# Kernel tuning notes

Hardware: AMD Instinct MI355X
Metric: run time of the kernel (lower is better)

Reference implementation:

```python
import jax, jax.numpy as jnp
import numpy as np

N = 20000   # nodes
E = 320000  # edges
F = 64      # input node features
H = 256     # hidden_layer_size
C = 10      # nbr_classes
G = 64      # graphs in the batch


def _lin(key, fan_in, fan_out):
    k1, k2 = jax.random.split(key)
    bound = 1.0 / np.sqrt(fan_in)
    W = jax.random.uniform(k1, (fan_in, fan_out), jnp.float32, -bound, bound)
    b = jax.random.uniform(k2, (fan_out,), jnp.float32, -bound, bound)
    return W, b


def setup_inputs() -> dict:
    key = jax.random.key(0)
    ks = jax.random.split(key, 10)
    x = jax.random.normal(ks[0], (N, F), jnp.float32)
    edge_index = jax.random.randint(ks[1], (2, E), 0, N)
    batch = jnp.sort(jax.random.randint(ks[2], (N,), 0, G))
    W1, b1 = _lin(ks[3], F, H)
    W2, b2 = _lin(ks[4], H, H)
    W3, b3 = _lin(ks[5], H, H)
    W4, b4 = _lin(ks[6], H, H)
    W5, b5 = _lin(ks[7], H, H)
    Wout, bout = _lin(ks[8], H, C)
    return {"x": x, "edge_index": edge_index, "batch": batch,
            "W1": W1, "b1": b1, "W2": W2, "b2": b2, "W3": W3, "b3": b3,
            "W4": W4, "b4": b4, "W5": W5, "b5": b5, "Wout": Wout, "bout": bout}


def reference(x, edge_index, batch, W1, b1, W2, b2, W3, b3, W4, b4, W5, b5, Wout, bout):
    # GCNConv (Kipf & Welling): add self-loops, D^{-1/2}(A+I)D^{-1/2} (X W) + b.
    # Dropout(p=0.5) is identity in eval mode (reference is deterministic).
    loop = jnp.arange(N)
    row = jnp.concatenate([edge_index[0], loop])  # source nodes, [E+N]
    col = jnp.concatenate([edge_index[1], loop])  # target nodes, [E+N]
    deg = jax.ops.segment_sum(jnp.ones(E + N, x.dtype), col, num_segments=N)
    dinv = jax.lax.rsqrt(deg)  # deg >= 1 thanks to self-loops
    norm = (dinv[row] * dinv[col])[:, None]  # [E+N, 1]

    def gcn_conv(h, W, b):
        m = (h @ W)[row] * norm                      # gather + normalize, [E+N, H]
        return jax.ops.segment_sum(m, col, num_segments=N) + b

    h = x
    for W, b in ((W1, b1), (W2, b2), (W3, b3), (W4, b4), (W5, b5)):
        h = jax.nn.relu(gcn_conv(h, W, b))

    # global_mean_pool over graph ids
    counts = jax.ops.segment_sum(jnp.ones(N, h.dtype), batch, num_segments=G)
    pooled = jax.ops.segment_sum(h, batch, num_segments=G) / jnp.maximum(counts, 1.0)[:, None]
    return pooled @ Wout + bout  # [G, C]
```

## Files before the change

kernel.cpp:

```cpp
#include <hip/hip_runtime.h>

#define NN 20000
#define NE 320000
#define FIN 64
#define HD 256
#define NC 10
#define NG 64
#define NB ((NN + 255) / 256)

typedef unsigned short u16;
typedef unsigned int u32;
typedef __attribute__((ext_vector_type(8))) short short8;
typedef __attribute__((ext_vector_type(4))) float f32x4;

__device__ __forceinline__ float bf2f(u16 u) {
    union { u32 i; float f; } v; v.i = ((u32)u) << 16; return v.f;
}
__device__ __forceinline__ u16 f2bf(float f) {
    union { float f; u32 i; } v; v.f = f;
    u32 r = v.i + 0x7fffu + ((v.i >> 16) & 1u);
    return (u16)(r >> 16);
}

__global__ void k_deg(const int* __restrict__ col, int* __restrict__ degi,
                      const int* __restrict__ batch, int* __restrict__ gstart) {
    int i = blockIdx.x * 256 + threadIdx.x;
    if (i < NE) atomicAdd(&degi[col[i]], 1);
    if (i < NN) {
        int b = batch[i];
        int prev = (i == 0) ? -1 : batch[i - 1];
        if (b != prev) gstart[b] = i;
    }
}

__global__ __launch_bounds__(256) void k_scan1(const int* __restrict__ degi,
                                               int* __restrict__ rowptr,
                                               int* __restrict__ bsum) {
    int t = threadIdx.x;
    int i = blockIdx.x * 256 + t;
    int v = (i < NN) ? degi[i] : 0;
    int lane = t & 63, wid = t >> 6;
    int x = v;
#pragma unroll
    for (int off = 1; off < 64; off <<= 1) {
        int y = __shfl_up(x, off);
        if (lane >= off) x += y;
    }
    __shared__ int ws[4];
    if (lane == 63) ws[wid] = x;
    __syncthreads();
    int woff = 0;
    for (int w = 0; w < wid; ++w) woff += ws[w];
    if (i < NN) rowptr[i] = woff + x - v;
    if (t == 255) bsum[blockIdx.x] = woff + x;
}

__global__ void k_scan3(const int* __restrict__ degi, const int* __restrict__ bsum,
                        int* __restrict__ rowptr, int* __restrict__ cursor,
                        float* __restrict__ dinv,
                        const float* __restrict__ x, u16* __restrict__ u0) {
    __shared__ int pref[NB];
    if (threadIdx.x < NB) pref[threadIdx.x] = bsum[threadIdx.x];
    __syncthreads();
    if (threadIdx.x == 0) {
        int run = 0;
        for (int k = 0; k < NB; ++k) { int t = pref[k]; pref[k] = run; run += t; }
    }
    __syncthreads();
    int i = blockIdx.x * 256 + threadIdx.x;
    if (i < NN) {
        int dg = degi[i];
        int rp = rowptr[i] + pref[i >> 8];
        rowptr[i] = rp;
        cursor[i] = rp;
        dinv[i] = rsqrtf((float)(1 + dg));
        if (i == NN - 1) rowptr[NN] = rp + dg;
    }
    if (i < NN * FIN / 4) {
        int node = i >> 4;
        float d = rsqrtf((float)(1 + degi[node]));
        float4 v = *(const float4*)&x[(size_t)i * 4];
        u32 lo = (u32)f2bf(v.x * d) | ((u32)f2bf(v.y * d) << 16);
        u32 hi = (u32)f2bf(v.z * d) | ((u32)f2bf(v.w * d) << 16);
        *(uint2*)&u0[(size_t)i * 4] = make_uint2(lo, hi);
    }
}

__global__ void k_fill(const int* __restrict__ row, const int* __restrict__ col,
                       int* __restrict__ cursor, int* __restrict__ ebuf) {
    int e = blockIdx.x * 256 + threadIdx.x;
    if (e < NE) {
        int c = col[e];
        int pos = atomicAdd(&cursor[c], 1);
        ebuf[pos] = row[e];
    }
}

__global__ __launch_bounds__(256) void k_trans(const float* __restrict__ W0, const float* __restrict__ W1,
                                               const float* __restrict__ W2, const float* __restrict__ W3,
                                               const float* __restrict__ W4,
                                               u16* __restrict__ T0, u16* __restrict__ T1,
                                               u16* __restrict__ T2, u16* __restrict__ T3,
                                               u16* __restrict__ T4) {
    int l = blockIdx.z;
    const float* W = (l == 0) ? W0 : (l == 1) ? W1 : (l == 2) ? W2 : (l == 3) ? W3 : W4;
    u16* T = (l == 0) ? T0 : (l == 1) ? T1 : (l == 2) ? T2 : (l == 3) ? T3 : T4;
    int K = (l == 0) ? FIN : HD;
    int k0 = blockIdx.x * 32;
    if (k0 >= K) return;
    int n0 = blockIdx.y * 32;
    __shared__ float tile[32][33];
    int tx = threadIdx.x & 31, ty = threadIdx.x >> 5;
#pragma unroll
    for (int r = 0; r < 32; r += 8)
        tile[ty + r][tx] = W[(size_t)(k0 + ty + r) * HD + n0 + tx];
    __syncthreads();
#pragma unroll
    for (int r = 0; r < 32; r += 8)
        T[(size_t)(n0 + ty + r) * K + k0 + tx] = f2bf(tile[tx][ty + r]);
}

__global__ __launch_bounds__(256) void k_gatherh(const u16* __restrict__ U,
                                                 const int* __restrict__ rowptr,
                                                 const int* __restrict__ ebuf,
                                                 const float* __restrict__ dinv,
                                                 u16* __restrict__ Z) {
    int b = blockIdx.x;
    int half = b & 1;
    int tile = b >> 1;
    int n = tile * 4 + (threadIdx.x >> 6);
    if (n >= NN) return;
    int lane = threadIdx.x & 63;
    int grp = lane >> 4;
    int seg = lane & 15;
    int fbase = half * 128 + seg * 8;
    int s = rowptr[n], e = rowptr[n + 1];
    float acc[8];
    if (grp == 0) {
        uint4 v = *(const uint4*)&U[(size_t)n * HD + fbase];
        acc[0] = bf2f((u16)(v.x & 0xffff)); acc[1] = bf2f((u16)(v.x >> 16));
        acc[2] = bf2f((u16)(v.y & 0xffff)); acc[3] = bf2f((u16)(v.y >> 16));
        acc[4] = bf2f((u16)(v.z & 0xffff)); acc[5] = bf2f((u16)(v.z >> 16));
        acc[6] = bf2f((u16)(v.w & 0xffff)); acc[7] = bf2f((u16)(v.w >> 16));
    } else {
#pragma unroll
        for (int k = 0; k < 8; ++k) acc[k] = 0.f;
    }
    for (int j = s; j < e; j += 16) {
        int idx = j + lane;
        int myid = (lane < 16 && idx < e) ? ebuf[idx] : -1;
        uint4 v[4];
#pragma unroll
        for (int k = 0; k < 4; ++k) {
            int r = __shfl(myid, grp * 4 + k);
            uint4 t = *(const uint4*)&U[(size_t)max(r, 0) * HD + fbase];
            if (r < 0) t = make_uint4(0u, 0u, 0u, 0u);
            v[k] = t;
        }
#pragma unroll
        for (int k = 0; k < 4; ++k) {
            acc[0] += bf2f((u16)(v[k].x & 0xffff)); acc[1] += bf2f((u16)(v[k].x >> 16));
            acc[2] += bf2f((u16)(v[k].y & 0xffff)); acc[3] += bf2f((u16)(v[k].y >> 16));
            acc[4] += bf2f((u16)(v[k].z & 0xffff)); acc[5] += bf2f((u16)(v[k].z >> 16));
            acc[6] += bf2f((u16)(v[k].w & 0xffff)); acc[7] += bf2f((u16)(v[k].w >> 16));
        }
    }
#pragma unroll
    for (int k = 0; k < 8; ++k) {
        acc[k] += __shfl_xor(acc[k], 16);
        acc[k] += __shfl_xor(acc[k], 32);
    }
    if (grp == 0) {
        float d = dinv[n];
        uint4 o;
        o.x = (u32)f2bf(acc[0] * d) | ((u32)f2bf(acc[1] * d) << 16);
        o.y = (u32)f2bf(acc[2] * d) | ((u32)f2bf(acc[3] * d) << 16);
        o.z = (u32)f2bf(acc[4] * d) | ((u32)f2bf(acc[5] * d) << 16);
        o.w = (u32)f2bf(acc[6] * d) | ((u32)f2bf(acc[7] * d) << 16);
        *(uint4*)&Z[(size_t)n * HD + fbase] = o;
    }
}

__global__ __launch_bounds__(256) void k_gather64(const u16* __restrict__ U,
                                                  const int* __restrict__ rowptr,
                                                  const int* __restrict__ ebuf,
                                                  const float* __restrict__ dinv,
                                                  u16* __restrict__ Z) {
    int n = blockIdx.x * 4 + (threadIdx.x >> 6);
    if (n >= NN) return;
    int lane = threadIdx.x & 63;
    int grp = lane >> 3;
    int seg = lane & 7;
    int s = rowptr[n], e = rowptr[n + 1];
    float acc[8];
    if (grp == 0) {
        uint4 v = *(const uint4*)&U[(size_t)n * FIN + seg * 8];
        acc[0] = bf2f((u16)(v.x & 0xffff)); acc[1] = bf2f((u16)(v.x >> 16));
        acc[2] = bf2f((u16)(v.y & 0xffff)); acc[3] = bf2f((u16)(v.y >> 16));
        acc[4] = bf2f((u16)(v.z & 0xffff)); acc[5] = bf2f((u16)(v.z >> 16));
        acc[6] = bf2f((u16)(v.w & 0xffff)); acc[7] = bf2f((u16)(v.w >> 16));
    } else {
#pragma unroll
        for (int k = 0; k < 8; ++k) acc[k] = 0.f;
    }
    for (int j = s; j < e; j += 16) {
        int i0 = j + grp, i1 = j + 8 + grp;
        int r0 = (i0 < e) ? ebuf[i0] : -1;
        int r1 = (i1 < e) ? ebuf[i1] : -1;
        uint4 v0 = *(const uint4*)&U[(size_t)max(r0, 0) * FIN + seg * 8];
        uint4 v1 = *(const uint4*)&U[(size_t)max(r1, 0) * FIN + seg * 8];
        if (r0 < 0) v0 = make_uint4(0u, 0u, 0u, 0u);
        if (r1 < 0) v1 = make_uint4(0u, 0u, 0u, 0u);
        acc[0] += bf2f((u16)(v0.x & 0xffff)); acc[1] += bf2f((u16)(v0.x >> 16));
        acc[2] += bf2f((u16)(v0.y & 0xffff)); acc[3] += bf2f((u16)(v0.y >> 16));
        acc[4] += bf2f((u16)(v0.z & 0xffff)); acc[5] += bf2f((u16)(v0.z >> 16));
        acc[6] += bf2f((u16)(v0.w & 0xffff)); acc[7] += bf2f((u16)(v0.w >> 16));
        acc[0] += bf2f((u16)(v1.x & 0xffff)); acc[1] += bf2f((u16)(v1.x >> 16));
        acc[2] += bf2f((u16)(v1.y & 0xffff)); acc[3] += bf2f((u16)(v1.y >> 16));
        acc[4] += bf2f((u16)(v1.z & 0xffff)); acc[5] += bf2f((u16)(v1.z >> 16));
        acc[6] += bf2f((u16)(v1.w & 0xffff)); acc[7] += bf2f((u16)(v1.w >> 16));
    }
#pragma unroll
    for (int off = 8; off < 64; off <<= 1)
#pragma unroll
        for (int k = 0; k < 8; ++k) acc[k] += __shfl_xor(acc[k], off);
    if (grp == 0) {
        float d = dinv[n];
        uint4 o;
        o.x = (u32)f2bf(acc[0] * d) | ((u32)f2bf(acc[1] * d) << 16);
        o.y = (u32)f2bf(acc[2] * d) | ((u32)f2bf(acc[3] * d) << 16);
        o.z = (u32)f2bf(acc[4] * d) | ((u32)f2bf(acc[5] * d) << 16);
        o.w = (u32)f2bf(acc[6] * d) | ((u32)f2bf(acc[7] * d) << 16);
        *(uint4*)&Z[(size_t)n * FIN + seg * 8] = o;
    }
}

__global__ __launch_bounds__(256) void k_mm(const u16* __restrict__ A,
                                            const u16* __restrict__ Wt,
                                            const float* __restrict__ bias,
                                            const float* __restrict__ dinv,
                                            u16* __restrict__ O,
                                            int K, int scaleOut) {
    __shared__ u16 Asm[64][40];
    __shared__ u16 Bsm[256][40];
    __shared__ float bs[HD];
    const int m0 = blockIdx.x * 64;
    const int t = threadIdx.x;
    const int wave = t >> 6;
    const int lane = t & 63;
    const int quad = lane >> 4;
    const int l16 = lane & 15;
    const int n0 = wave * 64;
    bs[t] = bias[t];

    f32x4 acc[4][4];
#pragma unroll
    for (int i = 0; i < 4; ++i)
#pragma unroll
        for (int j = 0; j < 4; ++j) acc[i][j] = (f32x4){0.f, 0.f, 0.f, 0.f};

    for (int k0 = 0; k0 < K; k0 += 32) {
        {
            int row = t >> 2, seg = t & 3;
            int gm = m0 + row;
            float4 v = make_float4(0.f, 0.f, 0.f, 0.f);
            if (gm < NN) v = *(const float4*)&A[(size_t)gm * K + k0 + seg * 8];
            *(float4*)&Asm[row][seg * 8] = v;
        }
        {
#pragma unroll
            for (int j = 0; j < 4; ++j) {
                float4 v = *(const float4*)&Wt[(size_t)t * K + k0 + j * 8];
                *(float4*)&Bsm[t][j * 8] = v;
            }
        }
        __syncthreads();
        short8 a[4], b[4];
#pragma unroll
        for (int i = 0; i < 4; ++i) a[i] = *(const short8*)&Asm[i * 16 + l16][quad * 8];
#pragma unroll
        for (int j = 0; j < 4; ++j) b[j] = *(const short8*)&Bsm[n0 + j * 16 + l16][quad * 8];
#pragma unroll
        for (int i = 0; i < 4; ++i)
#pragma unroll
            for (int j = 0; j < 4; ++j)
                acc[i][j] = __builtin_amdgcn_mfma_f32_16x16x32_bf16(a[i], b[j], acc[i][j], 0, 0, 0);
        __syncthreads();
    }
#pragma unroll
    for (int i = 0; i < 4; ++i) {
#pragma unroll
        for (int r = 0; r < 4; ++r) {
            int m = m0 + i * 16 + quad * 4 + r;
            if (m >= NN) continue;
            float d = scaleOut ? dinv[m] : 1.0f;
#pragma unroll
            for (int j = 0; j < 4; ++j) {
                int n = n0 + j * 16 + l16;
                float val = fmaxf(acc[i][j][r] + bs[n], 0.f) * d;
                O[(size_t)m * HD + n] = f2bf(val);
            }
        }
    }
}

__global__ __launch_bounds__(256) void k_poolout(const u16* __restrict__ h,
                                                 const int* __restrict__ gstart,
                                                 const float* __restrict__ Wout,
                                                 const float* __restrict__ bout,
                                                 float* __restrict__ out) {
    int g = blockIdx.x;
    int t = threadIdx.x;
    __shared__ float pooled[HD];
    __shared__ float part[NC][16];
    __shared__ int s_se[2];
    if (t == 0) {
        int st = gstart[g];
        int en = NN;
        for (int gg = g + 1; gg < NG; ++gg) en = min(en, gstart[gg]);
        s_se[0] = st; s_se[1] = en;
    }
    __syncthreads();
    int st = s_se[0], en = s_se[1];
    float a0 = 0.f, a1 = 0.f, a2 = 0.f, a3 = 0.f;
    int n = st;
    for (; n + 4 <= en; n += 4) {
        a0 += bf2f(h[(size_t)n * HD + t]);
        a1 += bf2f(h[(size_t)(n + 1) * HD + t]);
        a2 += bf2f(h[(size_t)(n + 2) * HD + t]);
        a3 += bf2f(h[(size_t)(n + 3) * HD + t]);
    }
    for (; n < en; ++n) a0 += bf2f(h[(size_t)n * HD + t]);
    float inv = 1.0f / (float)max(en - st, 1);
    pooled[t] = (a0 + a1 + a2 + a3) * inv;
    __syncthreads();
    if (t < NC * 16) {
        int c = t >> 4, l16 = t & 15;
        float s = 0.f;
        for (int f = l16; f < HD; f += 16)
            s = fmaf(pooled[f], Wout[(size_t)f * NC + c], s);
        part[c][l16] = s;
    }
    __syncthreads();
    if (t < NC) {
        float s = 0.f;
#pragma unroll
        for (int k = 0; k < 16; ++k) s += part[t][k];
        out[(size_t)g * NC + t] = s + bout[t];
    }
}

extern "C" void kernel_launch(void* const* d_in, const int* in_sizes, int n_in,
                              void* d_out, int out_size, void* d_ws, size_t ws_size,
                              hipStream_t stream) {
    const float* x     = (const float*)d_in[0];
    const int*   ei    = (const int*)d_in[1];
    const int*   batch = (const int*)d_in[2];
    const float* Wl[5] = {(const float*)d_in[3], (const float*)d_in[5], (const float*)d_in[7],
                          (const float*)d_in[9], (const float*)d_in[11]};
    const float* bl[5] = {(const float*)d_in[4], (const float*)d_in[6], (const float*)d_in[8],
                          (const float*)d_in[10], (const float*)d_in[12]};
    const float* Wout = (const float*)d_in[13];
    const float* bout = (const float*)d_in[14];
    float* out = (float*)d_out;

    const int* row = ei;
    const int* col = ei + NE;

    char* p = (char*)d_ws;
    auto take = [&](size_t bytes) { char* q = p; p += (bytes + 255) & ~(size_t)255; return q; };
    float* dinv   = (float*)take(NN * 4);
    int*   degi   = (int*)take(NN * 4);
    int*   rowptr = (int*)take((NN + 1) * 4);
    int*   cursor = (int*)take(NN * 4);
    int*   bsum   = (int*)take(NB * 4);
    int*   ebuf   = (int*)take(NE * 4);
    int*   gstart = (int*)take(NG * 4);
    u16*   Wt[5];
    for (int l = 0; l < 5; ++l) Wt[l] = (u16*)take((size_t)HD * HD * 2);
    u16*   B1     = (u16*)take((size_t)NN * HD * 2);
    u16*   B2     = (u16*)take((size_t)NN * HD * 2);

    hipMemsetAsync(degi, 0, NN * 4, stream);
    hipMemsetAsync(gstart, 0x7F, NG * 4, stream);
    k_deg<<<(NE + 255) / 256, 256, 0, stream>>>(col, degi, batch, gstart);
    k_scan1<<<NB, 256, 0, stream>>>(degi, rowptr, bsum);
    k_scan3<<<(NN * FIN / 4 + 255) / 256, 256, 0, stream>>>(degi, bsum, rowptr, cursor, dinv, x, B1);
    k_fill<<<(NE + 255) / 256, 256, 0, stream>>>(row, col, cursor, ebuf);
    dim3 tGrid(8, 8, 5);
    k_trans<<<tGrid, 256, 0, stream>>>(Wl[0], Wl[1], Wl[2], Wl[3], Wl[4],
                                       Wt[0], Wt[1], Wt[2], Wt[3], Wt[4]);

    k_gather64<<<(NN + 3) / 4, 256, 0, stream>>>(B1, rowptr, ebuf, dinv, B2);
    k_mm<<<(NN + 63) / 64, 256, 0, stream>>>(B2, Wt[0], bl[0], dinv, B1, FIN, 1);
    const int gGrid = 2 * ((NN + 3) / 4);
    for (int l = 1; l < 5; ++l) {
        k_gatherh<<<gGrid, 256, 0, stream>>>(B1, rowptr, ebuf, dinv, B2);
        k_mm<<<(NN + 63) / 64, 256, 0, stream>>>(B2, Wt[l], bl[l], dinv, B1, HD, (l < 4) ? 1 : 0);
    }

    k_poolout<<<NG, 256, 0, stream>>>(B1, gstart, Wout, bout, out);
}
```

Before: 350.4 us.

## Pad CSR rows to multiples of 16 with a zero sentinel node and store indices as u16

Each node's neighbour list is padded to a multiple of 16 and filled with a sentinel index (NN = 20000) that points to an extra zero row appended to each feature buffer. This removes the per-edge bounds checks and zero-selects in the gather kernels. Edge indices are also stored as 16-bit values, halving index traffic. In exchange there are extra padded gather loads of the zero row, an extra padding kernel, and a reliance on NN fitting in 16 bits.

```diff
diff --git a/kernel.cpp b/kernel.cpp
--- a/kernel.cpp
+++ b/kernel.cpp
@@ -7,6 +7,7 @@
 #define NC 10
 #define NG 64
 #define NB ((NN + 255) / 256)
+#define EBMAX (NE + 15 * NN + 16)
 
 typedef unsigned short u16;
 typedef unsigned int u32;
@@ -33,12 +34,17 @@
     }
 }
 
+__global__ void k_pad(u32* __restrict__ ebuf32) {
+    int i = blockIdx.x * 256 + threadIdx.x;
+    if (i < EBMAX / 2) ebuf32[i] = 0x4E204E20u;
+}
+
 __global__ __launch_bounds__(256) void k_scan1(const int* __restrict__ degi,
                                                int* __restrict__ rowptr,
                                                int* __restrict__ bsum) {
     int t = threadIdx.x;
     int i = blockIdx.x * 256 + t;
-    int v = (i < NN) ? degi[i] : 0;
+    int v = (i < NN) ? ((degi[i] + 15) & ~15) : 0;
     int lane = t & 63, wid = t >> 6;
     int x = v;
 #pragma unroll
@@ -74,7 +80,7 @@
         rowptr[i] = rp;
         cursor[i] = rp;
         dinv[i] = rsqrtf((float)(1 + dg));
-        if (i == NN - 1) rowptr[NN] = rp + dg;
+        if (i == NN - 1) rowptr[NN] = rp + ((dg + 15) & ~15);
     }
     if (i < NN * FIN / 4) {
         int node = i >> 4;
@@ -84,15 +90,16 @@
         u32 hi = (u32)f2bf(v.z * d) | ((u32)f2bf(v.w * d) << 16);
         *(uint2*)&u0[(size_t)i * 4] = make_uint2(lo, hi);
     }
+    if (blockIdx.x == 0 && threadIdx.x < FIN) u0[(size_t)NN * FIN + threadIdx.x] = 0;
 }
 
 __global__ void k_fill(const int* __restrict__ row, const int* __restrict__ col,
-                       int* __restrict__ cursor, int* __restrict__ ebuf) {
+                       int* __restrict__ cursor, u16* __restrict__ ebuf) {
     int e = blockIdx.x * 256 + threadIdx.x;
     if (e < NE) {
         int c = col[e];
         int pos = atomicAdd(&cursor[c], 1);
-        ebuf[pos] = row[e];
+        ebuf[pos] = (u16)row[e];
     }
 }
 
@@ -122,7 +129,7 @@
 
 __global__ __launch_bounds__(256) void k_gatherh(const u16* __restrict__ U,
                                                  const int* __restrict__ rowptr,
-                                                 const int* __restrict__ ebuf,
+                                                 const u16* __restrict__ ebuf,
                                                  const float* __restrict__ dinv,
                                                  u16* __restrict__ Z) {
     int b = blockIdx.x;
@@ -147,15 +154,12 @@
         for (int k = 0; k < 8; ++k) acc[k] = 0.f;
     }
     for (int j = s; j < e; j += 16) {
-        int idx = j + lane;
-        int myid = (lane < 16 && idx < e) ? ebuf[idx] : -1;
+        int myid = (lane < 16) ? (int)ebuf[j + lane] : 0;
         uint4 v[4];
 #pragma unroll
         for (int k = 0; k < 4; ++k) {
             int r = __shfl(myid, grp * 4 + k);
-            uint4 t = *(const uint4*)&U[(size_t)max(r, 0) * HD + fbase];
-            if (r < 0) t = make_uint4(0u, 0u, 0u, 0u);
-            v[k] = t;
+            v[k] = *(const uint4*)&U[(size_t)r * HD + fbase];
         }
 #pragma unroll
         for (int k = 0; k < 4; ++k) {
@@ -183,7 +187,7 @@
 
 __global__ __launch_bounds__(256) void k_gather64(const u16* __restrict__ U,
                                                   const int* __restrict__ rowptr,
-                                                  const int* __restrict__ ebuf,
+                                                  const u16* __restrict__ ebuf,
                                                   const float* __restrict__ dinv,
                                                   u16* __restrict__ Z) {
     int n = blockIdx.x * 4 + (threadIdx.x >> 6);
@@ -204,13 +208,10 @@
         for (int k = 0; k < 8; ++k) acc[k] = 0.f;
     }
     for (int j = s; j < e; j += 16) {
-        int i0 = j + grp, i1 = j + 8 + grp;
-        int r0 = (i0 < e) ? ebuf[i0] : -1;
-        int r1 = (i1 < e) ? ebuf[i1] : -1;
-        uint4 v0 = *(const uint4*)&U[(size_t)max(r0, 0) * FIN + seg * 8];
-        uint4 v1 = *(const uint4*)&U[(size_t)max(r1, 0) * FIN + seg * 8];
-        if (r0 < 0) v0 = make_uint4(0u, 0u, 0u, 0u);
-        if (r1 < 0) v1 = make_uint4(0u, 0u, 0u, 0u);
+        int r0 = (int)ebuf[j + grp];
+        int r1 = (int)ebuf[j + 8 + grp];
+        uint4 v0 = *(const uint4*)&U[(size_t)r0 * FIN + seg * 8];
+        uint4 v1 = *(const uint4*)&U[(size_t)r1 * FIN + seg * 8];
         acc[0] += bf2f((u16)(v0.x & 0xffff)); acc[1] += bf2f((u16)(v0.x >> 16));
         acc[2] += bf2f((u16)(v0.y & 0xffff)); acc[3] += bf2f((u16)(v0.y >> 16));
         acc[4] += bf2f((u16)(v0.z & 0xffff)); acc[5] += bf2f((u16)(v0.z >> 16));
@@ -252,6 +253,7 @@
     const int l16 = lane & 15;
     const int n0 = wave * 64;
     bs[t] = bias[t];
+    if (blockIdx.x == 0) O[(size_t)NN * HD + t] = 0;
 
     f32x4 acc[4][4];
 #pragma unroll
@@ -374,16 +376,17 @@
     int*   rowptr = (int*)take((NN + 1) * 4);
     int*   cursor = (int*)take(NN * 4);
     int*   bsum   = (int*)take(NB * 4);
-    int*   ebuf   = (int*)take(NE * 4);
+    u16*   ebuf   = (u16*)take(EBMAX * 2);
     int*   gstart = (int*)take(NG * 4);
     u16*   Wt[5];
     for (int l = 0; l < 5; ++l) Wt[l] = (u16*)take((size_t)HD * HD * 2);
-    u16*   B1     = (u16*)take((size_t)NN * HD * 2);
-    u16*   B2     = (u16*)take((size_t)NN * HD * 2);
+    u16*   B1     = (u16*)take((size_t)(NN + 1) * HD * 2);
+    u16*   B2     = (u16*)take((size_t)(NN + 1) * HD * 2);
 
     hipMemsetAsync(degi, 0, NN * 4, stream);
     hipMemsetAsync(gstart, 0x7F, NG * 4, stream);
     k_deg<<<(NE + 255) / 256, 256, 0, stream>>>(col, degi, batch, gstart);
+    k_pad<<<(EBMAX / 2 + 255) / 256, 256, 0, stream>>>((u32*)ebuf);
     k_scan1<<<NB, 256, 0, stream>>>(degi, rowptr, bsum);
     k_scan3<<<(NN * FIN / 4 + 255) / 256, 256, 0, stream>>>(degi, bsum, rowptr, cursor, dinv, x, B1);
     k_fill<<<(NE + 255) / 256, 256, 0, stream>>>(row, col, cursor, ebuf);
```

Result: no change. 347.7 us (-0.8%).
